# Kernel optimization log

Hardware: AMD Instinct MI355X
Metric: run time of the kernel (lower is better)

## Reference

```python
import jax, jax.numpy as jnp
import numpy as np


def setup_inputs() -> dict:
    key = jax.random.key(0)
    ks = jax.random.split(key, 7)
    S, A, I, H = 2000, 1000, 5, 32
    return {
        "g": jax.random.normal(ks[0], (S, A, I), dtype=jnp.float32),
        "W1": jax.random.normal(ks[1], (A, I, H), dtype=jnp.float32) * (1.0 / np.sqrt(I)),
        "b1": jax.random.normal(ks[2], (A, H), dtype=jnp.float32) * 0.01,
        "W2": jax.random.normal(ks[3], (A, H, H), dtype=jnp.float32) * (1.0 / np.sqrt(H)),
        "b2": jax.random.normal(ks[4], (A, H), dtype=jnp.float32) * 0.01,
        "W3": jax.random.normal(ks[5], (A, H, 1), dtype=jnp.float32) * (1.0 / np.sqrt(H)),
        "b3": jax.random.normal(ks[6], (A, 1), dtype=jnp.float32) * 0.01,
    }


def reference(g, W1, b1, W2, b2, W3, b3):
    # Batched equivalent of the nested per-struct / per-atom Python loop:
    # each atom `a` has its own tiny MLP (5 -> 32 -> 32 -> 1, tanh),
    # applied to g[s, a] for every structure s. Grouped-GEMM form:
    # s = struct, a = atom, i/h/o = feature dims.
    h1 = jnp.tanh(jnp.einsum('sai,aih->sah', g, W1) + b1[None, :, :])
    h2 = jnp.tanh(jnp.einsum('sah,aho->sao', h1, W2) + b2[None, :, :])
    e = jnp.einsum('sah,aho->sao', h2, W3) + b3[None, :, :]
    # e_nn has shape [n_struct, n_atoms], matching the torch buffer.
    return e[..., 0]
```

## Files before the change

kernel.cpp:

```cpp
#include <hip/hip_runtime.h>
#include <hip/hip_bf16.h>

#define NS_TOT 2000
#define NA 1000
#define NI 5
#define NH 32
#define SHALF 1000

typedef __attribute__((ext_vector_type(2)))  float f32x2;
typedef __attribute__((ext_vector_type(8)))  short short8;
typedef __attribute__((ext_vector_type(16))) float f32x16;

struct f4pair  { f32x2 a, b; };
struct accpair { f32x2 p[8]; };

__device__ __forceinline__ f32x2 tanh_pk(f32x2 X) {
    f32x2 z = X * X;
    f32x2 n = (z + 105.0f) * z + 945.0f;
    f32x2 d = (z * 15.0f + 420.0f) * z + 945.0f;
    f32x2 r;
    r.x = __builtin_amdgcn_rcpf(d.x);
    r.y = __builtin_amdgcn_rcpf(d.y);
    f32x2 t = X * n * r;
    t.x = __builtin_amdgcn_fmed3f(t.x, -1.0f, 1.0f);
    t.y = __builtin_amdgcn_fmed3f(t.y, -1.0f, 1.0f);
    return t;
}

__device__ __forceinline__ float4 ffma4(float s, float4 w, float4 acc) {
    acc.x = fmaf(s, w.x, acc.x);
    acc.y = fmaf(s, w.y, acc.y);
    acc.z = fmaf(s, w.z, acc.z);
    acc.w = fmaf(s, w.w, acc.w);
    return acc;
}

__device__ __forceinline__ unsigned short f2bf_rne(float x) {
    unsigned u = __float_as_uint(x);
    unsigned r = u + 0x7FFFu + ((u >> 16) & 1u);
    return (unsigned short)(r >> 16);
}

__device__ __forceinline__ unsigned pack2(float a, float b) {
    __hip_bfloat162 p = __float22bfloat162_rn(make_float2(a, b));
    unsigned u; __builtin_memcpy(&u, &p, 4); return u;
}

__global__ __attribute__((amdgpu_flat_work_group_size(256, 256),
                          amdgpu_waves_per_eu(4, 8)))
void mlp_mfma(
    const float* __restrict__ g,
    const float* __restrict__ W1, const float* __restrict__ b1,
    const float* __restrict__ W2, const float* __restrict__ b2,
    const float* __restrict__ W3, const float* __restrict__ b3,
    float* __restrict__ out)
{
    const int bid   = blockIdx.x;
    const int araw  = bid % NA;
    const int chunk = bid / NA;
    const int a = (araw >> 3) + 125 * (araw & 7);
    const int t = threadIdx.x;
    const int lane = t & 63, wid = t >> 6;
    const int l31 = lane & 31, half = lane >> 5;

    const int sbase_blk = chunk * SHALF;
    const int send      = sbase_blk + SHALF;

    __shared__ __align__(16) unsigned short sW2T[NH * NH];
    __shared__ __align__(16) float sB2[NH];
    __shared__ __align__(16) float sW3[NH];
    __shared__ __align__(16) unsigned short sH[4][64 * 40];

    for (int idx = t; idx < NH * NH; idx += 256) {
        const int i = idx >> 5, j = idx & 31;
        sW2T[j * NH + i] = f2bf_rne(W2[(size_t)a * NH * NH + idx]);
    }
    if (t < NH) { sB2[t] = b2[a * NH + t]; sW3[t] = W3[a * NH + t]; }
    __syncthreads();

    const short8 af0 = __builtin_bit_cast(short8, *(const uint4*)(sW2T + l31 * NH + half * 8));
    const short8 af1 = __builtin_bit_cast(short8, *(const uint4*)(sW2T + l31 * NH + 16 + half * 8));
    const float4 b2q0 = ((const float4*)sB2)[0 + half];
    const float4 b2q1 = ((const float4*)sB2)[2 + half];
    const float4 b2q2 = ((const float4*)sB2)[4 + half];
    const float4 b2q3 = ((const float4*)sB2)[6 + half];
    const float4 w3q0 = ((const float4*)sW3)[0 + half];
    const float4 w3q1 = ((const float4*)sW3)[2 + half];
    const float4 w3q2 = ((const float4*)sW3)[4 + half];
    const float4 w3q3 = ((const float4*)sW3)[6 + half];
    const float bias3 = b3[a];

    const f4pair w3p0 = __builtin_bit_cast(f4pair, w3q0);
    const f4pair w3p1 = __builtin_bit_cast(f4pair, w3q1);
    const f4pair w3p2 = __builtin_bit_cast(f4pair, w3q2);
    const f4pair w3p3 = __builtin_bit_cast(f4pair, w3q3);

    const float4* w1v = (const float4*)(W1 + (size_t)a * NI * NH);
    const float4* b1v = (const float4*)(b1 + (size_t)a * NH);

    unsigned short* hrow = sH[wid];

    for (int it = 0; it < 4; ++it) {
        const int base = sbase_blk + it * 256 + wid * 64;
        const int s = base + lane;
        const int sl = (s < send) ? s : (send - 1);

        const float* gp = g + ((size_t)sl * NA + a) * NI;
        const float x0g = gp[0], x1g = gp[1], x2g = gp[2], x3g = gp[3], x4g = gp[4];

        float4 h[8];
        #define INITH(q) h[q] = b1v[q];
        INITH(0) INITH(1) INITH(2) INITH(3) INITH(4) INITH(5) INITH(6) INITH(7)
        #undef INITH
        #define L1Q(i, q) h[q] = ffma4(xi, w1v[(i) * 8 + (q)], h[q]);
        #define L1I(i, xv) { const float xi = (xv); \
            L1Q(i,0) L1Q(i,1) L1Q(i,2) L1Q(i,3) L1Q(i,4) L1Q(i,5) L1Q(i,6) L1Q(i,7) }
        L1I(0, x0g) L1I(1, x1g) L1I(2, x2g) L1I(3, x3g) L1I(4, x4g)
        #undef L1I
        #undef L1Q

        f32x2 th[16];
        #define TH(q) { f4pair hp = __builtin_bit_cast(f4pair, h[q]); \
            th[2*(q)]   = tanh_pk(hp.a); \
            th[2*(q)+1] = tanh_pk(hp.b); }
        TH(0) TH(1) TH(2) TH(3) TH(4) TH(5) TH(6) TH(7)
        #undef TH

        uint4* wp = (uint4*)(hrow + lane * 40);
        wp[0] = make_uint4(pack2(th[0].x,th[0].y), pack2(th[1].x,th[1].y),
                           pack2(th[2].x,th[2].y), pack2(th[3].x,th[3].y));
        wp[1] = make_uint4(pack2(th[4].x,th[4].y), pack2(th[5].x,th[5].y),
                           pack2(th[6].x,th[6].y), pack2(th[7].x,th[7].y));
        wp[2] = make_uint4(pack2(th[8].x,th[8].y), pack2(th[9].x,th[9].y),
                           pack2(th[10].x,th[10].y), pack2(th[11].x,th[11].y));
        wp[3] = make_uint4(pack2(th[12].x,th[12].y), pack2(th[13].x,th[13].y),
                           pack2(th[14].x,th[14].y), pack2(th[15].x,th[15].y));
        __builtin_amdgcn_wave_barrier();

        const unsigned short* rb = hrow + half * 8;
        const short8 b00 = __builtin_bit_cast(short8, *(const uint4*)(rb + l31 * 40));
        const short8 b01 = __builtin_bit_cast(short8, *(const uint4*)(rb + l31 * 40 + 16));
        const short8 b10 = __builtin_bit_cast(short8, *(const uint4*)(rb + (32 + l31) * 40));
        const short8 b11 = __builtin_bit_cast(short8, *(const uint4*)(rb + (32 + l31) * 40 + 16));

        f32x16 acc0 = {b2q0.x, b2q0.y, b2q0.z, b2q0.w,
                       b2q1.x, b2q1.y, b2q1.z, b2q1.w,
                       b2q2.x, b2q2.y, b2q2.z, b2q2.w,
                       b2q3.x, b2q3.y, b2q3.z, b2q3.w};
        f32x16 acc1 = acc0;
        acc0 = __builtin_amdgcn_mfma_f32_32x32x16_bf16(af0, b00, acc0, 0, 0, 0);
        acc0 = __builtin_amdgcn_mfma_f32_32x32x16_bf16(af1, b01, acc0, 0, 0, 0);
        acc1 = __builtin_amdgcn_mfma_f32_32x32x16_bf16(af0, b10, acc1, 0, 0, 0);
        acc1 = __builtin_amdgcn_mfma_f32_32x32x16_bf16(af1, b11, acc1, 0, 0, 0);

        const accpair ap0 = __builtin_bit_cast(accpair, acc0);
        const accpair ap1 = __builtin_bit_cast(accpair, acc1);
        f32x2 p0 = {0.f, 0.f}, p1 = {0.f, 0.f};
        #define EPP(r, wpair) { \
            p0 += tanh_pk(ap0.p[r]) * (wpair); \
            p1 += tanh_pk(ap1.p[r]) * (wpair); }
        EPP(0, w3p0.a) EPP(1, w3p0.b)
        EPP(2, w3p1.a) EPP(3, w3p1.b)
        EPP(4, w3p2.a) EPP(5, w3p2.b)
        EPP(6, w3p3.a) EPP(7, w3p3.b)
        #undef EPP
        float e0 = p0.x + p0.y;
        float e1 = p1.x + p1.y;
        e0 += __shfl_xor(e0, 32);
        e1 += __shfl_xor(e1, 32);

        if (lane < 32) {
            const int st0 = base + l31;
            const int st1 = base + 32 + l31;
            if (st0 < send) out[(size_t)st0 * NA + a] = e0 + bias3;
            if (st1 < send) out[(size_t)st1 * NA + a] = e1 + bias3;
        }
    }
}

extern "C" void kernel_launch(void* const* d_in, const int* in_sizes, int n_in,
                              void* d_out, int out_size, void* d_ws, size_t ws_size,
                              hipStream_t stream) {
    const float* g  = (const float*)d_in[0];
    const float* W1 = (const float*)d_in[1];
    const float* b1 = (const float*)d_in[2];
    const float* W2 = (const float*)d_in[3];
    const float* b2 = (const float*)d_in[4];
    const float* W3 = (const float*)d_in[5];
    const float* b3 = (const float*)d_in[6];
    float* out = (float*)d_out;
    mlp_mfma<<<dim3(NA * 2), dim3(256), 0, stream>>>(g, W1, b1, W2, b2, W3, b3, out);
}
```

Before: 137.0 us.

## Compute layer 1 with MFMA and pass activations via lane shuffles instead of LDS

Layer 1 (5->32 plus bias) now runs as a bf16 MFMA. W1 and b1 are packed into a padded 8-wide bf16 tile, and the input is augmented with a constant 1 so the bias folds into the matmul. The tanh outputs in the MFMA accumulator layout are rearranged into the B-operand layout for layer 2 with cross-half shuffles, which removes the per-wave LDS staging buffer and its wave barrier. The aim is to cut scalar FMA work and LDS traffic. In exchange, layer 1 inputs, weights and bias are now rounded to bf16, which lowers accuracy, and more shuffle and select instructions are added.

```diff
diff --git a/kernel.cpp b/kernel.cpp
--- a/kernel.cpp
+++ b/kernel.cpp
@@ -14,6 +14,14 @@
 struct f4pair  { f32x2 a, b; };
 struct accpair { f32x2 p[8]; };
 
+__device__ __forceinline__ float fast_tanh(float x) {
+    float z = x * x;
+    float n = fmaf(z + 105.0f, z, 945.0f);
+    float d = fmaf(fmaf(z, 15.0f, 420.0f), z, 945.0f);
+    float r = __builtin_amdgcn_rcpf(d);
+    float tv = x * n * r;
+    return __builtin_amdgcn_fmed3f(tv, -1.0f, 1.0f);
+}
 __device__ __forceinline__ f32x2 tanh_pk(f32x2 X) {
     f32x2 z = X * X;
     f32x2 n = (z + 105.0f) * z + 945.0f;
@@ -27,20 +35,11 @@
     return t;
 }
 
-__device__ __forceinline__ float4 ffma4(float s, float4 w, float4 acc) {
-    acc.x = fmaf(s, w.x, acc.x);
-    acc.y = fmaf(s, w.y, acc.y);
-    acc.z = fmaf(s, w.z, acc.z);
-    acc.w = fmaf(s, w.w, acc.w);
-    return acc;
-}
-
 __device__ __forceinline__ unsigned short f2bf_rne(float x) {
     unsigned u = __float_as_uint(x);
     unsigned r = u + 0x7FFFu + ((u >> 16) & 1u);
     return (unsigned short)(r >> 16);
 }
-
 __device__ __forceinline__ unsigned pack2(float a, float b) {
     __hip_bfloat162 p = __float22bfloat162_rn(make_float2(a, b));
     unsigned u; __builtin_memcpy(&u, &p, 4); return u;
@@ -67,17 +66,30 @@
     const int send      = sbase_blk + SHALF;
 
     __shared__ __align__(16) unsigned short sW2T[NH * NH];
+    __shared__ __align__(16) unsigned short sW1T[NH * 8];
     __shared__ __align__(16) float sB2[NH];
     __shared__ __align__(16) float sW3[NH];
-    __shared__ __align__(16) unsigned short sH[4][64 * 40];
 
     for (int idx = t; idx < NH * NH; idx += 256) {
         const int i = idx >> 5, j = idx & 31;
         sW2T[j * NH + i] = f2bf_rne(W2[(size_t)a * NH * NH + idx]);
     }
-    if (t < NH) { sB2[t] = b2[a * NH + t]; sW3[t] = W3[a * NH + t]; }
+    if (t < NH) {
+        sB2[t] = b2[a * NH + t];
+        sW3[t] = W3[a * NH + t];
+        const int m = t;
+        #pragma unroll
+        for (int i = 0; i < NI; ++i)
+            sW1T[m * 8 + i] = f2bf_rne(W1[(size_t)a * NI * NH + i * NH + m]);
+        sW1T[m * 8 + 5] = f2bf_rne(b1[a * NH + m]);
+        sW1T[m * 8 + 6] = 0;
+        sW1T[m * 8 + 7] = 0;
+    }
     __syncthreads();
 
+    const short8 zero8 = {0,0,0,0,0,0,0,0};
+    const short8 w1ld = __builtin_bit_cast(short8, *(const uint4*)(sW1T + l31 * 8));
+    const short8 afl1 = half ? zero8 : w1ld;
     const short8 af0 = __builtin_bit_cast(short8, *(const uint4*)(sW2T + l31 * NH + half * 8));
     const short8 af1 = __builtin_bit_cast(short8, *(const uint4*)(sW2T + l31 * NH + 16 + half * 8));
     const float4 b2q0 = ((const float4*)sB2)[0 + half];
@@ -89,16 +101,11 @@
     const float4 w3q2 = ((const float4*)sW3)[4 + half];
     const float4 w3q3 = ((const float4*)sW3)[6 + half];
     const float bias3 = b3[a];
-
     const f4pair w3p0 = __builtin_bit_cast(f4pair, w3q0);
     const f4pair w3p1 = __builtin_bit_cast(f4pair, w3q1);
     const f4pair w3p2 = __builtin_bit_cast(f4pair, w3q2);
     const f4pair w3p3 = __builtin_bit_cast(f4pair, w3q3);
-
-    const float4* w1v = (const float4*)(W1 + (size_t)a * NI * NH);
-    const float4* b1v = (const float4*)(b1 + (size_t)a * NH);
-
-    unsigned short* hrow = sH[wid];
+    const f32x16 zacc = {0,0,0,0,0,0,0,0,0,0,0,0,0,0,0,0};
 
     for (int it = 0; it < 4; ++it) {
         const int base = sbase_blk + it * 256 + wid * 64;
@@ -108,50 +115,71 @@
         const float* gp = g + ((size_t)sl * NA + a) * NI;
         const float x0g = gp[0], x1g = gp[1], x2g = gp[2], x3g = gp[3], x4g = gp[4];
 
-        float4 h[8];
-        #define INITH(q) h[q] = b1v[q];
-        INITH(0) INITH(1) INITH(2) INITH(3) INITH(4) INITH(5) INITH(6) INITH(7)
-        #undef INITH
-        #define L1Q(i, q) h[q] = ffma4(xi, w1v[(i) * 8 + (q)], h[q]);
-        #define L1I(i, xv) { const float xi = (xv); \
-            L1Q(i,0) L1Q(i,1) L1Q(i,2) L1Q(i,3) L1Q(i,4) L1Q(i,5) L1Q(i,6) L1Q(i,7) }
-        L1I(0, x0g) L1I(1, x1g) L1I(2, x2g) L1I(3, x3g) L1I(4, x4g)
-        #undef L1I
-        #undef L1Q
-
-        f32x2 th[16];
-        #define TH(q) { f4pair hp = __builtin_bit_cast(f4pair, h[q]); \
-            th[2*(q)]   = tanh_pk(hp.a); \
-            th[2*(q)+1] = tanh_pk(hp.b); }
-        TH(0) TH(1) TH(2) TH(3) TH(4) TH(5) TH(6) TH(7)
-        #undef TH
-
-        uint4* wp = (uint4*)(hrow + lane * 40);
-        wp[0] = make_uint4(pack2(th[0].x,th[0].y), pack2(th[1].x,th[1].y),
-                           pack2(th[2].x,th[2].y), pack2(th[3].x,th[3].y));
-        wp[1] = make_uint4(pack2(th[4].x,th[4].y), pack2(th[5].x,th[5].y),
-                           pack2(th[6].x,th[6].y), pack2(th[7].x,th[7].y));
-        wp[2] = make_uint4(pack2(th[8].x,th[8].y), pack2(th[9].x,th[9].y),
-                           pack2(th[10].x,th[10].y), pack2(th[11].x,th[11].y));
-        wp[3] = make_uint4(pack2(th[12].x,th[12].y), pack2(th[13].x,th[13].y),
-                           pack2(th[14].x,th[14].y), pack2(th[15].x,th[15].y));
-        __builtin_amdgcn_wave_barrier();
-
-        const unsigned short* rb = hrow + half * 8;
-        const short8 b00 = __builtin_bit_cast(short8, *(const uint4*)(rb + l31 * 40));
-        const short8 b01 = __builtin_bit_cast(short8, *(const uint4*)(rb + l31 * 40 + 16));
-        const short8 b10 = __builtin_bit_cast(short8, *(const uint4*)(rb + (32 + l31) * 40));
-        const short8 b11 = __builtin_bit_cast(short8, *(const uint4*)(rb + (32 + l31) * 40 + 16));
+        const unsigned gp01 = pack2(x0g, x1g);
+        const unsigned gp23 = pack2(x2g, x3g);
+        const unsigned gp45 = pack2(x4g, 1.0f);
+        const unsigned q01 = __shfl_xor((int)gp01, 32);
+        const unsigned q23 = __shfl_xor((int)gp23, 32);
+        const unsigned q45 = __shfl_xor((int)gp45, 32);
+        const unsigned zu = 0;
+        uint4 bu0 = make_uint4(half ? zu : gp01, half ? zu : gp23,
+                               half ? zu : gp45, zu);
+        uint4 bu1 = make_uint4(half ? zu : q01, half ? zu : q23,
+                               half ? zu : q45, zu);
+        const short8 gb0 = __builtin_bit_cast(short8, bu0);
+        const short8 gb1 = __builtin_bit_cast(short8, bu1);
+
+        f32x16 d0 = __builtin_amdgcn_mfma_f32_32x32x16_bf16(afl1, gb0, zacc, 0, 0, 0);
+        f32x16 d1 = __builtin_amdgcn_mfma_f32_32x32x16_bf16(afl1, gb1, zacc, 0, 0, 0);
+
+        short8 bk0_0, bk1_0, bk0_1, bk1_1;
+        #define TILE_CONV(DD, BK0, BK1) { \
+            float th[16]; \
+            th[0]=fast_tanh(DD[0]);   th[1]=fast_tanh(DD[1]); \
+            th[2]=fast_tanh(DD[2]);   th[3]=fast_tanh(DD[3]); \
+            th[4]=fast_tanh(DD[4]);   th[5]=fast_tanh(DD[5]); \
+            th[6]=fast_tanh(DD[6]);   th[7]=fast_tanh(DD[7]); \
+            th[8]=fast_tanh(DD[8]);   th[9]=fast_tanh(DD[9]); \
+            th[10]=fast_tanh(DD[10]); th[11]=fast_tanh(DD[11]); \
+            th[12]=fast_tanh(DD[12]); th[13]=fast_tanh(DD[13]); \
+            th[14]=fast_tanh(DD[14]); th[15]=fast_tanh(DD[15]); \
+            float rc[8]; \
+            rc[0] = __shfl_xor(half ? th[0]  : th[4],  32); \
+            rc[1] = __shfl_xor(half ? th[1]  : th[5],  32); \
+            rc[2] = __shfl_xor(half ? th[2]  : th[6],  32); \
+            rc[3] = __shfl_xor(half ? th[3]  : th[7],  32); \
+            rc[4] = __shfl_xor(half ? th[8]  : th[12], 32); \
+            rc[5] = __shfl_xor(half ? th[9]  : th[13], 32); \
+            rc[6] = __shfl_xor(half ? th[10] : th[14], 32); \
+            rc[7] = __shfl_xor(half ? th[11] : th[15], 32); \
+            float e0[8], e1[8]; \
+            e0[0] = half ? rc[0] : th[0]; e0[1] = half ? rc[1] : th[1]; \
+            e0[2] = half ? rc[2] : th[2]; e0[3] = half ? rc[3] : th[3]; \
+            e0[4] = half ? th[4] : rc[0]; e0[5] = half ? th[5] : rc[1]; \
+            e0[6] = half ? th[6] : rc[2]; e0[7] = half ? th[7] : rc[3]; \
+            e1[0] = half ? rc[4] : th[8];  e1[1] = half ? rc[5] : th[9]; \
+            e1[2] = half ? rc[6] : th[10]; e1[3] = half ? rc[7] : th[11]; \
+            e1[4] = half ? th[12] : rc[4]; e1[5] = half ? th[13] : rc[5]; \
+            e1[6] = half ? th[14] : rc[6]; e1[7] = half ? th[15] : rc[7]; \
+            uint4 u0 = make_uint4(pack2(e0[0],e0[1]), pack2(e0[2],e0[3]), \
+                                  pack2(e0[4],e0[5]), pack2(e0[6],e0[7])); \
+            uint4 u1 = make_uint4(pack2(e1[0],e1[1]), pack2(e1[2],e1[3]), \
+                                  pack2(e1[4],e1[5]), pack2(e1[6],e1[7])); \
+            BK0 = __builtin_bit_cast(short8, u0); \
+            BK1 = __builtin_bit_cast(short8, u1); }
+        TILE_CONV(d0, bk0_0, bk1_0)
+        TILE_CONV(d1, bk0_1, bk1_1)
+        #undef TILE_CONV
 
         f32x16 acc0 = {b2q0.x, b2q0.y, b2q0.z, b2q0.w,
                        b2q1.x, b2q1.y, b2q1.z, b2q1.w,
                        b2q2.x, b2q2.y, b2q2.z, b2q2.w,
                        b2q3.x, b2q3.y, b2q3.z, b2q3.w};
         f32x16 acc1 = acc0;
-        acc0 = __builtin_amdgcn_mfma_f32_32x32x16_bf16(af0, b00, acc0, 0, 0, 0);
-        acc0 = __builtin_amdgcn_mfma_f32_32x32x16_bf16(af1, b01, acc0, 0, 0, 0);
-        acc1 = __builtin_amdgcn_mfma_f32_32x32x16_bf16(af0, b10, acc1, 0, 0, 0);
-        acc1 = __builtin_amdgcn_mfma_f32_32x32x16_bf16(af1, b11, acc1, 0, 0, 0);
+        acc0 = __builtin_amdgcn_mfma_f32_32x32x16_bf16(af0, bk0_0, acc0, 0, 0, 0);
+        acc0 = __builtin_amdgcn_mfma_f32_32x32x16_bf16(af1, bk1_0, acc0, 0, 0, 0);
+        acc1 = __builtin_amdgcn_mfma_f32_32x32x16_bf16(af0, bk0_1, acc1, 0, 0, 0);
+        acc1 = __builtin_amdgcn_mfma_f32_32x32x16_bf16(af1, bk1_1, acc1, 0, 0, 0);
 
         const accpair ap0 = __builtin_bit_cast(accpair, acc0);
         const accpair ap1 = __builtin_bit_cast(accpair, acc1);
```

Result: slower. 156.2 us (+14.0%).
